# Kernel tuning notes

Hardware: AMD Instinct MI355X
Metric: run time of the kernel (lower is better)

Reference implementation:

```python
import jax, jax.numpy as jnp
import numpy as np

D_MODEL = 1024
N_HEADS = 16
D_K = D_MODEL // N_HEADS
THETA = 10000.0
BATCH = 1
SEQ = 4096


def setup_inputs() -> dict:
    key = jax.random.key(0)
    ks = jax.random.split(key, 5)
    std = (2.0 / (D_MODEL + D_MODEL)) ** 0.5
    mk = lambda k: jax.random.truncated_normal(k, -3.0, 3.0, (D_MODEL, D_MODEL), jnp.float32) * std
    return {
        "x": jax.random.normal(ks[0], (BATCH, SEQ, D_MODEL), jnp.float32),
        "Wq": mk(ks[1]),
        "Wk": mk(ks[2]),
        "Wv": mk(ks[3]),
        "Wo": mk(ks[4]),
    }


def _rope(x, pos, inv_freq):
    # x: [b, h, s, d_k]; pos: [s]; inv_freq: [d_k/2]
    angles = pos[:, None].astype(jnp.float32) * inv_freq  # [s, d_k/2]
    cos = jnp.repeat(jnp.cos(angles), 2, axis=-1)  # [s, d_k]
    sin = jnp.repeat(jnp.sin(angles), 2, axis=-1)
    # interleaved rotation: (-x1, x0, -x3, x2, ...)
    x_rot = jnp.stack([-x[..., 1::2], x[..., 0::2]], axis=-1).reshape(x.shape)
    return x * cos + x_rot * sin


def reference(x, Wq, Wk, Wv, Wo):
    b, s, _ = x.shape
    h, dk = N_HEADS, D_K
    proj = lambda W: jnp.einsum('bsi,oi->bso', x, W).reshape(b, s, h, dk).transpose(0, 2, 1, 3)
    q = proj(Wq)
    k = proj(Wk)
    v = proj(Wv)
    pos = jnp.arange(s)
    inv_freq = 1.0 / THETA ** (jnp.arange(0, dk, 2, dtype=jnp.float32) / dk)
    q = _rope(q, pos, inv_freq)
    k = _rope(k, pos, inv_freq)
    scores = jnp.einsum('bhqd,bhkd->bhqk', q, k) / jnp.sqrt(jnp.asarray(dk, jnp.float32))
    causal_mask = jnp.arange(s)[None, :] > jnp.arange(s)[:, None]  # [s, s], True above diag
    scores = jnp.where(causal_mask, -jnp.inf, scores)
    weights = jax.nn.softmax(scores, axis=-1)
    out = jnp.einsum('bhqk,bhkd->bhqd', weights, v)
    out = out.transpose(0, 2, 1, 3).reshape(b, s, h * dk)
    return jnp.einsum('bsi,oi->bso', out, Wo)
```

## Files before the change

### kernel.cpp

```cpp
#include <hip/hip_runtime.h>
#include <hip/hip_bf16.h>


typedef __hip_bfloat16 bf16;
using s16x4 = __attribute__((ext_vector_type(4))) short;
using s16x8 = __attribute__((ext_vector_type(8))) short;
using f32x4 = __attribute__((ext_vector_type(4))) float;

#define SEQ 4096
#define DMODEL 1024
#define NHEADS 16
#define DK 64
#define LOG2_THETA 13.287712379549449f
#define SCALE_LOG2E 0.1803368801111244f

__device__ __forceinline__ void async16(const bf16* g, bf16* l) {
  __builtin_amdgcn_global_load_lds(
      (const __attribute__((address_space(1))) unsigned int*)g,
      (__attribute__((address_space(3))) unsigned int*)l, 16, 0, 0);
}

__global__ __launch_bounds__(256)
void conv_kernel(const float* __restrict__ s0, const float* __restrict__ s1,
                 const float* __restrict__ s2, const float* __restrict__ s3,
                 const float* __restrict__ s4,
                 bf16* __restrict__ d0, bf16* __restrict__ d1,
                 bf16* __restrict__ d2, bf16* __restrict__ d3,
                 bf16* __restrict__ d4) {
  const int z = blockIdx.z;
  const float* s = (z == 0) ? s0 : (z == 1) ? s1 : (z == 2) ? s2 : (z == 3) ? s3 : s4;
  bf16* d = (z == 0) ? d0 : (z == 1) ? d1 : (z == 2) ? d2 : (z == 3) ? d3 : d4;
  const int n = (z == 0) ? SEQ * DMODEL : DMODEL * DMODEL;
  const int i = (blockIdx.x * 256 + threadIdx.x) * 8;
  if (i >= n) return;
  const float4 a = *(const float4*)(s + i);
  const float4 b = *(const float4*)(s + i + 4);
  union { bf16 h[8]; s16x8 v; } u;
  u.h[0] = __float2bfloat16(a.x); u.h[1] = __float2bfloat16(a.y);
  u.h[2] = __float2bfloat16(a.z); u.h[3] = __float2bfloat16(a.w);
  u.h[4] = __float2bfloat16(b.x); u.h[5] = __float2bfloat16(b.y);
  u.h[6] = __float2bfloat16(b.z); u.h[7] = __float2bfloat16(b.w);
  *(s16x8*)(d + i) = u.v;
}

__global__ __launch_bounds__(256)
void gemm_kernel(const bf16* __restrict__ A,
                 const bf16* __restrict__ W0, const bf16* __restrict__ W1,
                 const bf16* __restrict__ W2,
                 bf16* __restrict__ D0, bf16* __restrict__ D1,
                 bf16* __restrict__ D2, float* __restrict__ Df,
                 int mode_base) {
  const int mode = mode_base + (int)blockIdx.z;
  const bf16* __restrict__ W = (mode == 1) ? W1 : (mode == 2) ? W2 : W0;
  bf16* __restrict__ D = (mode == 1) ? D1 : (mode == 2) ? D2 : D0;

  const int tid  = threadIdx.x;
  const int lane = tid & 63;
  const int wave = tid >> 6;
  const int wm = wave >> 1, wn = wave & 1;
  const int quad = lane >> 4, l16 = lane & 15;
  const int m0 = blockIdx.x * 128;
  const int n0 = blockIdx.y * 128;

  __shared__ __align__(16) bf16 As[128 * 32];
  __shared__ __align__(16) bf16 Bs[128 * 32];
  __shared__ __align__(16) bf16 Es[4][64 * 64];

  f32x4 acc[4][4] = {};

  const int ldrow = lane >> 2;
  const int ldcol = (lane & 3) * 8;

  for (int k0 = 0; k0 < DMODEL; k0 += 32) {
#pragma unroll
    for (int c = 0; c < 2; ++c) {
      const int chunk = wave * 2 + c;
      const int row = chunk * 16 + ldrow;
      async16(&A[(size_t)(m0 + row) * DMODEL + k0 + ldcol], &As[chunk * 512]);
      async16(&W[(size_t)(n0 + row) * DMODEL + k0 + ldcol], &Bs[chunk * 512]);
    }
    __syncthreads();

    s16x8 af[4], bfr[4];
#pragma unroll
    for (int i = 0; i < 4; ++i)
      af[i] = *(const s16x8*)&As[(wm * 64 + i * 16 + l16) * 32 + quad * 8];
#pragma unroll
    for (int j = 0; j < 4; ++j)
      bfr[j] = *(const s16x8*)&Bs[(wn * 64 + j * 16 + l16) * 32 + quad * 8];
#pragma unroll
    for (int i = 0; i < 4; ++i)
#pragma unroll
      for (int j = 0; j < 4; ++j)
        acc[i][j] = __builtin_amdgcn_mfma_f32_16x16x32_bf16(af[i], bfr[j],
                                                            acc[i][j], 0, 0, 0);
    __syncthreads();
  }

  if (mode == 3) {
#pragma unroll
    for (int i = 0; i < 4; ++i)
#pragma unroll
      for (int j = 0; j < 4; ++j) {
        const int col = n0 + wn * 64 + j * 16 + l16;
#pragma unroll
        for (int r = 0; r < 4; ++r) {
          const int srow = m0 + wm * 64 + i * 16 + quad * 4 + r;
          Df[(size_t)srow * DMODEL + col] = acc[i][j][r];
        }
      }
    return;
  }

  if (mode == 2) {
#pragma unroll
    for (int i = 0; i < 4; ++i)
#pragma unroll
      for (int j = 0; j < 4; ++j)
#pragma unroll
        for (int r = 0; r < 4; ++r)
          Es[wave][(j * 16 + l16) * 64 + i * 16 + quad * 4 + r] =
              __float2bfloat16(acc[i][j][r]);
  } else {
#pragma unroll
    for (int i = 0; i < 4; ++i)
#pragma unroll
      for (int j = 0; j < 4; ++j)
#pragma unroll
        for (int r = 0; r < 4; ++r)
          Es[wave][(i * 16 + quad * 4 + r) * 64 + j * 16 + l16] =
              __float2bfloat16(acc[i][j][r]);
  }
  __syncthreads();

  const int h = (n0 >> 6) + wn;
  const int g  = lane >> 3;
  const int c8 = (lane & 7) * 8;

  if (mode == 2) {
#pragma unroll
    for (int t = 0; t < 8; ++t) {
      const int d = t * 8 + g;
      const s16x8 v = *(const s16x8*)&Es[wave][d * 64 + c8];
      *(s16x8*)&D[((size_t)h * DK + d) * SEQ + m0 + wm * 64 + c8] = v;
    }
  } else {
    const float qs = (mode == 0) ? SCALE_LOG2E : 1.0f;
    float sn[4], cs[4], s8[4], c8r[4], invf[4];
    const int srow0 = m0 + wm * 64 + g;
#pragma unroll
    for (int k = 0; k < 4; ++k) {
      const int p = (c8 >> 1) + k;
      invf[k] = __builtin_amdgcn_exp2f((float)p * (-2.0f / 64.0f) * LOG2_THETA);
      sincosf((float)srow0 * invf[k], &sn[k], &cs[k]);
      sincosf(8.0f * invf[k], &s8[k], &c8r[k]);
      sn[k] *= qs; cs[k] *= qs;
    }
#pragma unroll
    for (int t = 0; t < 8; ++t) {
      const int rl = t * 8 + g;
      union { bf16 h[8]; s16x8 v; } u, o;
      u.v = *(const s16x8*)&Es[wave][rl * 64 + c8];
#pragma unroll
      for (int k = 0; k < 4; ++k) {
        const float x0 = __bfloat162float(u.h[2 * k]);
        const float x1 = __bfloat162float(u.h[2 * k + 1]);
        o.h[2 * k]     = __float2bfloat16(x0 * cs[k] - x1 * sn[k]);
        o.h[2 * k + 1] = __float2bfloat16(x1 * cs[k] + x0 * sn[k]);
        const float ns_ = sn[k] * c8r[k] + cs[k] * s8[k];
        cs[k] = cs[k] * c8r[k] - sn[k] * s8[k];
        sn[k] = ns_;
      }
      const int srow = m0 + wm * 64 + rl;
      *(s16x8*)&D[((size_t)h * SEQ + srow) * DK + c8] = o.v;
    }
  }
}

__global__ __launch_bounds__(256, 4)
void attn_kernel(const bf16* __restrict__ Q, const bf16* __restrict__ K,
                 const bf16* __restrict__ Vt, bf16* __restrict__ O) {
  const int tid  = threadIdx.x;
  const int lane = tid & 63;
  const int wave = tid >> 6;
  const int quad = lane >> 4, l16 = lane & 15;

  const int i  = (int)blockIdx.x;
  const int j  = i & 255;
  const int vv = 3 - (i >> 8);
  const int h  = j & 15;
  const int a  = j >> 4;
  const int qb = vv * 16 + ((vv & 1) ? (15 - a) : a);

  const bf16* __restrict__ Qh = Q + (size_t)h * SEQ * DK;
  const bf16* __restrict__ Kh = K + (size_t)h * SEQ * DK;
  const bf16* __restrict__ Vh = Vt + (size_t)h * DK * SEQ;

  __shared__ __align__(16) bf16 Ks[2][64 * 64];
  __shared__ __align__(16) bf16 Vs[2][64 * 64];
  __shared__ __align__(16) bf16 Pt[4][16 * 64];
  bf16* __restrict__ Ptw = Pt[wave];

  const short ONE = 0x3F80;
  const s16x8 ones = {ONE, ONE, ONE, ONE, ONE, ONE, ONE, ONE};

  const int srow = lane >> 3;
  const int schk = (lane & 7) ^ srow;
  const int xsw  = l16 & 7;
  const int xp   = (l16 & 7) << 3;

  const int q0 = qb * 64;
  const int qw = q0 + wave * 16;
  const int nb = qb + 1;

  const s16x8 aq0 = *(const s16x8*)&Qh[(size_t)(qw + l16) * DK + quad * 8];
  const s16x8 aq1 = *(const s16x8*)&Qh[(size_t)(qw + l16) * DK + 32 + quad * 8];

  f32x4 oacc[4] = {};
  f32x4 lacc = {};

  {
    const bf16* kg = Kh;
#pragma unroll
    for (int c = 0; c < 2; ++c) {
      const int chunk = wave * 2 + c;
      async16(kg + (size_t)(chunk * 8 + srow) * 64 + schk * 8,
              &Ks[0][chunk * 512]);
      async16(Vh + (size_t)(chunk * 8 + srow) * SEQ + schk * 8,
              &Vs[0][chunk * 512]);
    }
  }
  __syncthreads();

  for (int kb = 0; kb < nb; ++kb) {
    const int cur = kb & 1;
    if (kb + 1 < nb) {
      const int nxt = cur ^ 1;
      const int kv1 = (kb + 1) * 64;
      const bf16* kg = Kh + (size_t)kv1 * DK;
#pragma unroll
      for (int c = 0; c < 2; ++c) {
        const int chunk = wave * 2 + c;
        async16(kg + (size_t)(chunk * 8 + srow) * 64 + schk * 8,
                &Ks[nxt][chunk * 512]);
        async16(Vh + (size_t)(chunk * 8 + srow) * SEQ + kv1 + schk * 8,
                &Vs[nxt][chunk * 512]);
      }
    }

    f32x4 sc[4] = {};
    __builtin_amdgcn_s_setprio(1);
#pragma unroll
    for (int hh = 0; hh < 4; ++hh) {
      const bf16* kr = &Ks[cur][(hh * 16 + l16) * 64];
      const s16x8 ak0 = *(const s16x8*)&kr[(quad ^ xsw) * 8];
      const s16x8 ak1 = *(const s16x8*)&kr[((quad + 4) ^ xsw) * 8];
      sc[hh] = __builtin_amdgcn_mfma_f32_16x16x32_bf16(ak0, aq0, sc[hh], 0, 0, 0);
      sc[hh] = __builtin_amdgcn_mfma_f32_16x16x32_bf16(ak1, aq1, sc[hh], 0, 0, 0);
    }
    __builtin_amdgcn_s_setprio(0);

    if (kb == nb - 1) {
      const int lim = wave * 16 + l16 - quad * 4;
#pragma unroll
      for (int hh = 0; hh < 4; ++hh)
#pragma unroll
        for (int r = 0; r < 4; ++r)
          if (hh * 16 + r > lim) sc[hh][r] = -1e30f;
    }

#pragma unroll
    for (int hh = 0; hh < 4; ++hh) {
      union { bf16 b[4]; s16x4 v; } pk;
#pragma unroll
      for (int r = 0; r < 4; ++r)
        pk.b[r] = __float2bfloat16(__builtin_amdgcn_exp2f(sc[hh][r]));
      *(s16x4*)&Ptw[l16 * 64 + ((hh * 16 + quad * 4) ^ xp)] = pk.v;
    }
    const s16x8 ap0 = *(const s16x8*)&Ptw[l16 * 64 + ((quad * 8) ^ xp)];
    const s16x8 ap1 = *(const s16x8*)&Ptw[l16 * 64 + ((32 + quad * 8) ^ xp)];

    __builtin_amdgcn_s_setprio(1);
#pragma unroll
    for (int ns = 0; ns < 4; ++ns) {
      const bf16* vr = &Vs[cur][(ns * 16 + l16) * 64];
      const s16x8 bv0 = *(const s16x8*)&vr[(quad ^ xsw) * 8];
      const s16x8 bv1 = *(const s16x8*)&vr[((quad + 4) ^ xsw) * 8];
      oacc[ns] = __builtin_amdgcn_mfma_f32_16x16x32_bf16(ap0, bv0, oacc[ns], 0, 0, 0);
      oacc[ns] = __builtin_amdgcn_mfma_f32_16x16x32_bf16(ap1, bv1, oacc[ns], 0, 0, 0);
    }
    lacc = __builtin_amdgcn_mfma_f32_16x16x32_bf16(ap0, ones, lacc, 0, 0, 0);
    lacc = __builtin_amdgcn_mfma_f32_16x16x32_bf16(ap1, ones, lacc, 0, 0, 0);
    __builtin_amdgcn_s_setprio(0);

    __syncthreads();
  }

  float rl[4];
#pragma unroll
  for (int r = 0; r < 4; ++r) rl[r] = __builtin_amdgcn_rcpf(lacc[r]);
#pragma unroll
  for (int ns = 0; ns < 4; ++ns)
#pragma unroll
    for (int r = 0; r < 4; ++r) {
      const int row = quad * 4 + r;
      Ptw[row * 64 + ((ns * 16 + l16) ^ ((row & 7) << 3))] =
          __float2bfloat16(oacc[ns][r] * rl[r]);
    }
  const int g = lane >> 3, c8 = (lane & 7) * 8;
#pragma unroll
  for (int t = 0; t < 2; ++t) {
    const int row = t * 8 + g;
    const s16x8 v = *(const s16x8*)&Ptw[row * 64 + (c8 ^ ((row & 7) << 3))];
    *(s16x8*)&O[(size_t)(qw + row) * DMODEL + h * DK + c8] = v;
  }
}

extern "C" void kernel_launch(void* const* d_in, const int* in_sizes, int n_in,
                              void* d_out, int out_size, void* d_ws, size_t ws_size,
                              hipStream_t stream) {
  const float* x  = (const float*)d_in[0];
  const float* Wq = (const float*)d_in[1];
  const float* Wk = (const float*)d_in[2];
  const float* Wv = (const float*)d_in[3];
  const float* Wo = (const float*)d_in[4];
  float* out = (float*)d_out;

  bf16* ws = (bf16*)d_ws;
  bf16* xb   = ws;
  bf16* Wqb  = xb  + (size_t)SEQ * DMODEL;
  bf16* Wkb  = Wqb + (size_t)DMODEL * DMODEL;
  bf16* Wvb  = Wkb + (size_t)DMODEL * DMODEL;
  bf16* Wob  = Wvb + (size_t)DMODEL * DMODEL;
  bf16* Qb   = Wob + (size_t)DMODEL * DMODEL;
  bf16* Kb   = Qb  + (size_t)SEQ * DMODEL;
  bf16* Vtb  = Kb  + (size_t)SEQ * DMODEL;
  bf16* Attn = Vtb + (size_t)SEQ * DMODEL;

  conv_kernel<<<dim3(SEQ * DMODEL / (256 * 8), 1, 5), 256, 0, stream>>>(
      x, Wq, Wk, Wv, Wo, xb, Wqb, Wkb, Wvb, Wob);
  gemm_kernel<<<dim3(SEQ / 128, DMODEL / 128, 3), 256, 0, stream>>>(
      xb, Wqb, Wkb, Wvb, Qb, Kb, Vtb, out, 0);
  attn_kernel<<<dim3(64 * NHEADS), 256, 0, stream>>>(Qb, Kb, Vtb, Attn);
  gemm_kernel<<<dim3(SEQ / 128, DMODEL / 128, 1), 256, 0, stream>>>(
      Attn, Wob, Wob, Wob, Attn, Attn, Attn, out, 3);
}
```

Before: 218.9 us.

## Split attention waves 2x2 over queries and keys, keep P in registers

Attention waves are rearranged from four 16-query strips into a 2x2 grid. Each wave handles 32 queries against half of each 64-key block, so every K fragment read from LDS feeds two query groups. P is passed straight from the score MFMA output layout into 16x16x16 bf16 MFMAs for PV, which drops the per-wave LDS round trip for P. Row sums are now accumulated with scalar adds instead of an extra ones-MFMA. The cost is a cross-wave reduction of partial O and row sums through shared memory at the end, plus extra syncs and register pressure from doubled accumulators, under a launch bound of 4 blocks.

```diff
diff --git a/kernel.cpp b/kernel.cpp
--- a/kernel.cpp
+++ b/kernel.cpp
@@ -13,6 +13,22 @@
 #define DK 64
 #define LOG2_THETA 13.287712379549449f
 #define SCALE_LOG2E 0.1803368801111244f
+
+#if defined(__has_builtin)
+#if __has_builtin(__builtin_amdgcn_mfma_f32_16x16x16bf16_1k)
+#define HAVE_MFMA16 1
+#endif
+#endif
+
+__device__ __forceinline__ f32x4 mfma16(s16x4 a, s16x4 b, f32x4 c) {
+#ifdef HAVE_MFMA16
+  return __builtin_amdgcn_mfma_f32_16x16x16bf16_1k(a, b, c, 0, 0, 0);
+#else
+  asm volatile("v_mfma_f32_16x16x16_bf16 %0, %1, %2, %0"
+               : "+v"(c) : "v"(a), "v"(b));
+  return c;
+#endif
+}
 
 __device__ __forceinline__ void async16(const bf16* g, bf16* l) {
   __builtin_amdgcn_global_load_lds(
@@ -184,6 +200,8 @@
   const int lane = tid & 63;
   const int wave = tid >> 6;
   const int quad = lane >> 4, l16 = lane & 15;
+  const int wq = wave & 1;
+  const int wk = wave >> 1;
 
   const int i  = (int)blockIdx.x;
   const int j  = i & 255;
@@ -196,38 +214,38 @@
   const bf16* __restrict__ Kh = K + (size_t)h * SEQ * DK;
   const bf16* __restrict__ Vh = Vt + (size_t)h * DK * SEQ;
 
-  __shared__ __align__(16) bf16 Ks[2][64 * 64];
-  __shared__ __align__(16) bf16 Vs[2][64 * 64];
-  __shared__ __align__(16) bf16 Pt[4][16 * 64];
-  bf16* __restrict__ Ptw = Pt[wave];
-
-  const short ONE = 0x3F80;
-  const s16x8 ones = {ONE, ONE, ONE, ONE, ONE, ONE, ONE, ONE};
+  __shared__ __align__(16) char smemb[32768];
+  bf16* __restrict__ smem = (bf16*)smemb;
+  bf16* __restrict__ KsB = smem;
+  bf16* __restrict__ VsB = smem + 8192;
 
   const int srow = lane >> 3;
   const int schk = (lane & 7) ^ srow;
   const int xsw  = l16 & 7;
-  const int xp   = (l16 & 7) << 3;
 
   const int q0 = qb * 64;
-  const int qw = q0 + wave * 16;
+  const int qw = q0 + wq * 32;
   const int nb = qb + 1;
 
-  const s16x8 aq0 = *(const s16x8*)&Qh[(size_t)(qw + l16) * DK + quad * 8];
-  const s16x8 aq1 = *(const s16x8*)&Qh[(size_t)(qw + l16) * DK + 32 + quad * 8];
-
-  f32x4 oacc[4] = {};
-  f32x4 lacc = {};
+  s16x8 aq[2][2];
+#pragma unroll
+  for (int gq = 0; gq < 2; ++gq) {
+    const size_t qr = (size_t)(qw + gq * 16 + l16) * DK;
+    aq[gq][0] = *(const s16x8*)&Qh[qr + quad * 8];
+    aq[gq][1] = *(const s16x8*)&Qh[qr + 32 + quad * 8];
+  }
+
+  f32x4 oacc[2][4] = {};
+  float lsum[2] = {0.f, 0.f};
 
   {
-    const bf16* kg = Kh;
 #pragma unroll
     for (int c = 0; c < 2; ++c) {
       const int chunk = wave * 2 + c;
-      async16(kg + (size_t)(chunk * 8 + srow) * 64 + schk * 8,
-              &Ks[0][chunk * 512]);
+      async16(Kh + (size_t)(chunk * 8 + srow) * 64 + schk * 8,
+              &KsB[chunk * 512]);
       async16(Vh + (size_t)(chunk * 8 + srow) * SEQ + schk * 8,
-              &Vs[0][chunk * 512]);
+              &VsB[chunk * 512]);
     }
   }
   __syncthreads();
@@ -242,77 +260,134 @@
       for (int c = 0; c < 2; ++c) {
         const int chunk = wave * 2 + c;
         async16(kg + (size_t)(chunk * 8 + srow) * 64 + schk * 8,
-                &Ks[nxt][chunk * 512]);
+                &KsB[nxt * 4096 + chunk * 512]);
         async16(Vh + (size_t)(chunk * 8 + srow) * SEQ + kv1 + schk * 8,
-                &Vs[nxt][chunk * 512]);
-      }
-    }
-
-    f32x4 sc[4] = {};
+                &VsB[nxt * 4096 + chunk * 512]);
+      }
+    }
+
+    const bf16* __restrict__ Ksc = &KsB[cur * 4096];
+    const bf16* __restrict__ Vsc = &VsB[cur * 4096];
+
+    f32x4 sc[2][2] = {};
     __builtin_amdgcn_s_setprio(1);
 #pragma unroll
-    for (int hh = 0; hh < 4; ++hh) {
-      const bf16* kr = &Ks[cur][(hh * 16 + l16) * 64];
+    for (int hh = 0; hh < 2; ++hh) {
+      const bf16* kr = &Ksc[(wk * 32 + hh * 16 + l16) * 64];
       const s16x8 ak0 = *(const s16x8*)&kr[(quad ^ xsw) * 8];
       const s16x8 ak1 = *(const s16x8*)&kr[((quad + 4) ^ xsw) * 8];
-      sc[hh] = __builtin_amdgcn_mfma_f32_16x16x32_bf16(ak0, aq0, sc[hh], 0, 0, 0);
-      sc[hh] = __builtin_amdgcn_mfma_f32_16x16x32_bf16(ak1, aq1, sc[hh], 0, 0, 0);
+#pragma unroll
+      for (int gq = 0; gq < 2; ++gq) {
+        sc[gq][hh] = __builtin_amdgcn_mfma_f32_16x16x32_bf16(ak0, aq[gq][0], sc[gq][hh], 0, 0, 0);
+        sc[gq][hh] = __builtin_amdgcn_mfma_f32_16x16x32_bf16(ak1, aq[gq][1], sc[gq][hh], 0, 0, 0);
+      }
     }
     __builtin_amdgcn_s_setprio(0);
 
     if (kb == nb - 1) {
-      const int lim = wave * 16 + l16 - quad * 4;
-#pragma unroll
-      for (int hh = 0; hh < 4; ++hh)
+#pragma unroll
+      for (int gq = 0; gq < 2; ++gq) {
+        const int lim = wq * 32 + gq * 16 + l16 - wk * 32 - quad * 4;
+#pragma unroll
+        for (int hh = 0; hh < 2; ++hh)
+#pragma unroll
+          for (int r = 0; r < 4; ++r)
+            if (hh * 16 + r > lim) sc[gq][hh][r] = -1e30f;
+      }
+    }
+
+    s16x4 ap[2][2];
+#pragma unroll
+    for (int gq = 0; gq < 2; ++gq) {
+#pragma unroll
+      for (int hh = 0; hh < 2; ++hh) {
+        union { bf16 b[4]; s16x4 v; } pk;
+        float ps = 0.f;
+#pragma unroll
+        for (int r = 0; r < 4; ++r) {
+          const float p = __builtin_amdgcn_exp2f(sc[gq][hh][r]);
+          pk.b[r] = __float2bfloat16(p);
+          ps += p;
+        }
+        lsum[gq] += ps;
+        ap[gq][hh] = pk.v;
+      }
+    }
+
+    __builtin_amdgcn_s_setprio(1);
+#pragma unroll
+    for (int hh = 0; hh < 2; ++hh) {
+      const int cg = wk * 4 + hh * 2 + (quad >> 1);
+      const int eo = ((cg ^ xsw) << 3) + (quad & 1) * 4;
+#pragma unroll
+      for (int ns = 0; ns < 4; ++ns) {
+        const s16x4 bv = *(const s16x4*)&Vsc[(ns * 16 + l16) * 64 + eo];
+#pragma unroll
+        for (int gq = 0; gq < 2; ++gq)
+          oacc[gq][ns] = mfma16(ap[gq][hh], bv, oacc[gq][ns]);
+      }
+    }
+    __builtin_amdgcn_s_setprio(0);
+
+    __syncthreads();
+  }
+
+  float* __restrict__ Ored = (float*)smemb;
+  float* __restrict__ lred = (float*)(smemb + 16896);
+  bf16*  __restrict__ Obuf = (bf16*)(smemb + 17408);
+
+#pragma unroll
+  for (int gq = 0; gq < 2; ++gq) {
+    lsum[gq] += __shfl_xor(lsum[gq], 16);
+    lsum[gq] += __shfl_xor(lsum[gq], 32);
+  }
+
+  if (wk == 0) {
+    if (quad == 0)
+#pragma unroll
+      for (int gq = 0; gq < 2; ++gq)
+        lred[wq * 32 + gq * 16 + l16] = lsum[gq];
+  } else {
+#pragma unroll
+    for (int gq = 0; gq < 2; ++gq)
+#pragma unroll
+      for (int ns = 0; ns < 4; ++ns)
 #pragma unroll
         for (int r = 0; r < 4; ++r)
-          if (hh * 16 + r > lim) sc[hh][r] = -1e30f;
-    }
-
-#pragma unroll
-    for (int hh = 0; hh < 4; ++hh) {
-      union { bf16 b[4]; s16x4 v; } pk;
+          Ored[(wq * 32 + gq * 16 + quad * 4 + r) * 66 + ns * 16 + l16] =
+              oacc[gq][ns][r];
+  }
+  __syncthreads();
+  if (wk == 1 && quad == 0) {
+#pragma unroll
+    for (int gq = 0; gq < 2; ++gq)
+      lred[wq * 32 + gq * 16 + l16] += lsum[gq];
+  }
+  __syncthreads();
+  if (wk == 0) {
+#pragma unroll
+    for (int gq = 0; gq < 2; ++gq) {
+      float rl[4];
 #pragma unroll
       for (int r = 0; r < 4; ++r)
-        pk.b[r] = __float2bfloat16(__builtin_amdgcn_exp2f(sc[hh][r]));
-      *(s16x4*)&Ptw[l16 * 64 + ((hh * 16 + quad * 4) ^ xp)] = pk.v;
-    }
-    const s16x8 ap0 = *(const s16x8*)&Ptw[l16 * 64 + ((quad * 8) ^ xp)];
-    const s16x8 ap1 = *(const s16x8*)&Ptw[l16 * 64 + ((32 + quad * 8) ^ xp)];
-
-    __builtin_amdgcn_s_setprio(1);
-#pragma unroll
-    for (int ns = 0; ns < 4; ++ns) {
-      const bf16* vr = &Vs[cur][(ns * 16 + l16) * 64];
-      const s16x8 bv0 = *(const s16x8*)&vr[(quad ^ xsw) * 8];
-      const s16x8 bv1 = *(const s16x8*)&vr[((quad + 4) ^ xsw) * 8];
-      oacc[ns] = __builtin_amdgcn_mfma_f32_16x16x32_bf16(ap0, bv0, oacc[ns], 0, 0, 0);
-      oacc[ns] = __builtin_amdgcn_mfma_f32_16x16x32_bf16(ap1, bv1, oacc[ns], 0, 0, 0);
-    }
-    lacc = __builtin_amdgcn_mfma_f32_16x16x32_bf16(ap0, ones, lacc, 0, 0, 0);
-    lacc = __builtin_amdgcn_mfma_f32_16x16x32_bf16(ap1, ones, lacc, 0, 0, 0);
-    __builtin_amdgcn_s_setprio(0);
-
-    __syncthreads();
-  }
-
-  float rl[4];
-#pragma unroll
-  for (int r = 0; r < 4; ++r) rl[r] = __builtin_amdgcn_rcpf(lacc[r]);
-#pragma unroll
-  for (int ns = 0; ns < 4; ++ns)
-#pragma unroll
-    for (int r = 0; r < 4; ++r) {
-      const int row = quad * 4 + r;
-      Ptw[row * 64 + ((ns * 16 + l16) ^ ((row & 7) << 3))] =
-          __float2bfloat16(oacc[ns][r] * rl[r]);
-    }
-  const int g = lane >> 3, c8 = (lane & 7) * 8;
-#pragma unroll
-  for (int t = 0; t < 2; ++t) {
-    const int row = t * 8 + g;
-    const s16x8 v = *(const s16x8*)&Ptw[row * 64 + (c8 ^ ((row & 7) << 3))];
-    *(s16x8*)&O[(size_t)(qw + row) * DMODEL + h * DK + c8] = v;
+        rl[r] = __builtin_amdgcn_rcpf(lred[wq * 32 + gq * 16 + quad * 4 + r]);
+#pragma unroll
+      for (int ns = 0; ns < 4; ++ns)
+#pragma unroll
+        for (int r = 0; r < 4; ++r) {
+          const int row = wq * 32 + gq * 16 + quad * 4 + r;
+          const float v = oacc[gq][ns][r] + Ored[row * 66 + ns * 16 + l16];
+          Obuf[row * 72 + ns * 16 + l16] = __float2bfloat16(v * rl[r]);
+        }
+    }
+  }
+  __syncthreads();
+#pragma unroll
+  for (int p = 0; p < 2; ++p) {
+    const int row = p * 32 + (tid >> 3);
+    const int c8 = (tid & 7) * 8;
+    const s16x8 v = *(const s16x8*)&Obuf[row * 72 + c8];
+    *(s16x8*)&O[(size_t)(q0 + row) * DMODEL + h * DK + c8] = v;
   }
 }
 
```

Measured after the change: 208.1 us. 4.9% less time.
